# Kernel tuning notes

Hardware: AMD Instinct MI355X
Metric: run time of the kernel (lower is better)

## Reference

```python
import jax, jax.numpy as jnp
import numpy as np
from jax import lax

PS = 2  # patch_size
DN = ('NCHW', 'OIHW', 'NCHW')


def setup_inputs() -> dict:
    key = jax.random.key(0)
    ks = jax.random.split(key, 7)
    B, C, H, W = 8, 32, 512, 512
    return {
        'x': jax.random.normal(ks[0], (B, C, H, W), dtype=jnp.float32),
        'mlp_w': jax.random.normal(ks[1], (1, 1), dtype=jnp.float32),
        'mlp_b': jax.random.normal(ks[2], (1,), dtype=jnp.float32) * 0.1,
        'conv_w': jax.random.normal(ks[3], (C, 2 * C, 1, 1), dtype=jnp.float32) * (1.0 / np.sqrt(2 * C)),
        'conv_b': jax.random.normal(ks[4], (C,), dtype=jnp.float32) * 0.1,
        'convout_w': jax.random.normal(ks[5], (C, 2, 7, 7), dtype=jnp.float32) * (1.0 / np.sqrt(2 * 49)),
        'convout_b': jax.random.normal(ks[6], (C,), dtype=jnp.float32) * 0.1,
    }


def reference(x, mlp_w, mlp_b, conv_w, conv_b, convout_w, convout_b):
    B, C, H, W = x.shape
    hn, wn = H // PS, W // PS
    # Vectorized form of the per-patch Python loop:
    # blocks: (B, C, hn, PS, wn, PS)
    xb = x.reshape(B, C, hn, PS, wn, PS)
    m = jnp.max(xb, axis=(3, 5))   # (B, C, hn, wn) patch max pool
    a = jnp.mean(xb, axis=(3, 5))  # (B, C, hn, wn) patch avg pool
    # mlp(m) + mlp(a) with shared Linear(1,1): (m + a) * w + 2b
    gate = jax.nn.sigmoid((m + a) * mlp_w[0, 0] + 2.0 * mlp_b[0])
    product = (xb * gate[:, :, :, None, :, None]).reshape(B, C, H, W)
    # channel attention block
    cat = jnp.concatenate([product, x], axis=1)  # (B, 2C, H, W)
    out = lax.conv_general_dilated(cat, conv_w, (1, 1), 'SAME',
                                   dimension_numbers=DN) + conv_b[None, :, None, None]
    fs = out
    cm = jnp.max(out, axis=1, keepdims=True)   # channel max pool (B,1,H,W)
    ca = jnp.mean(out, axis=1, keepdims=True)  # channel avg pool (B,1,H,W)
    att = lax.conv_general_dilated(jnp.concatenate([cm, ca], axis=1), convout_w,
                                   (1, 1), 'SAME', dimension_numbers=DN)
    att = att + convout_b[None, :, None, None]
    return jax.nn.sigmoid(att) * fs
```

## Files before the change

### kernel.cpp

```cpp
#include <hip/hip_runtime.h>
#include <cstdint>
#include <cstddef>

constexpr int B = 8, C = 32, H = 512, W = 512;
constexpr int HW = H * W;

__device__ __forceinline__ float sigmoidf_(float z) {
    return 1.0f / (1.0f + __expf(-z));
}

__device__ __forceinline__ unsigned short bf16rne(float x) {
    unsigned int b = __float_as_uint(x);
    return (unsigned short)((b + 0x7FFFu + ((b >> 16) & 1u)) >> 16);
}
__device__ __forceinline__ float bf16tof(unsigned short h) {
    return __uint_as_float(((unsigned int)h) << 16);
}

typedef short s8v  __attribute__((ext_vector_type(8)));
typedef float f16v __attribute__((ext_vector_type(16)));

__global__ __launch_bounds__(256, 4) void k1_gate_conv(
    const float* __restrict__ x, const float* __restrict__ mlp_w,
    const float* __restrict__ mlp_b, const float* __restrict__ conv_w,
    const float* __restrict__ conv_b, float* __restrict__ fs,
    float* __restrict__ cm, float* __restrict__ ca)
{
    __shared__ float xs[32][256];
    __shared__ float gs[32][64];
    const int t  = threadIdx.x;
    const int c0 = blockIdx.x * 128;
    const int h0 = blockIdx.y * 2;
    const int b  = blockIdx.z;

    #pragma unroll
    for (int k = 0; k < 8; ++k) {
        int li = k * 256 + t;
        int c = li >> 6, q = li & 63;
        int p = q * 4;
        int row = p >> 7, col = p & 127;
        const float4 v = *(const float4*)(x + ((size_t)(b * C + c) * H + h0 + row) * W + c0 + col);
        *(float4*)&xs[c][p] = v;
    }
    __syncthreads();

    const float gw = mlp_w[0];
    const float gb = 2.0f * mlp_b[0];
    #pragma unroll
    for (int k = 0; k < 8; ++k) {
        int gi = k * 256 + t;
        int c = gi >> 6, wp = gi & 63;
        float a0 = xs[c][2 * wp],       a1 = xs[c][2 * wp + 1];
        float a2 = xs[c][128 + 2 * wp], a3 = xs[c][129 + 2 * wp];
        float mx = fmaxf(fmaxf(a0, a1), fmaxf(a2, a3));
        float av = 0.25f * ((a0 + a1) + (a2 + a3));
        gs[c][wp] = sigmoidf_(fmaf(mx + av, gw, gb));
    }
    __syncthreads();

    const int row = t >> 7, col = t & 127, wp = col >> 1;
    float xv[32], xg[32];
    #pragma unroll
    for (int c = 0; c < 32; ++c) {
        float v = xs[c][t];
        xv[c] = v;
        xg[c] = v * gs[c][wp];
    }
    float cmax = -3.4e38f, csum = 0.0f;
    const size_t pixoff = ((size_t)(b * C) * H + h0 + row) * W + c0 + col;
    #pragma unroll 4
    for (int o = 0; o < 32; ++o) {
        const float* wr = conv_w + o * 64;
        float acc0 = conv_b[o], acc1 = 0.0f;
        #pragma unroll
        for (int c = 0; c < 32; ++c) {
            acc0 = fmaf(xg[c], wr[c],      acc0);
            acc1 = fmaf(xv[c], wr[32 + c], acc1);
        }
        float acc = acc0 + acc1;
        fs[pixoff + (size_t)o * HW] = acc;
        cmax = fmaxf(cmax, acc);
        csum += acc;
    }
    const size_t pp = ((size_t)b * H + h0 + row) * W + c0 + col;
    cm[pp] = cmax;
    ca[pp] = csum * (1.0f / 32.0f);
}

__global__ __launch_bounds__(256, 3) void k2_conv7_mfma(
    const float* __restrict__ cm, const float* __restrict__ ca,
    const float* __restrict__ convout_w, const float* __restrict__ convout_b,
    float* __restrict__ io )
{
    __shared__ unsigned short win[4 * 14 * 144];
    const int t  = threadIdx.x;
    const int x0 = blockIdx.x * 128;
    const int y0 = blockIdx.y * 8;
    const int b  = blockIdx.z;

    #pragma unroll
    for (int k = 0; k < 16; ++k) {
        int n = k * 256 + t;
        if (n < 4032) {
            int j   = (n >= 2016) ? 1 : 0;
            int rem = n - j * 2016;
            int row = rem / 144;
            int col = rem - row * 144;
            int gy = y0 - 3 + row;
            int gx = x0 - 3 + col;
            float v = 0.0f;
            if ((unsigned)gy < (unsigned)H && (unsigned)gx < (unsigned)W)
                v = (j ? ca : cm)[(size_t)b * HW + (size_t)gy * W + gx];
            unsigned short hb = bf16rne(v);
            unsigned short lb = bf16rne(v - bf16tof(hb));
            win[n]        = hb;
            win[n + 4032] = lb;
        }
    }

    const int l  = t & 63;
    const int wv = t >> 6;
    const int o  = l & 31;
    const int j  = l >> 5;
    s8v whi[7], wlo[7];
    #pragma unroll
    for (int dy = 0; dy < 7; ++dy) {
        #pragma unroll
        for (int q = 0; q < 8; ++q) {
            float wf = (q < 7) ? convout_w[(o * 2 + j) * 49 + dy * 7 + q] : 0.0f;
            unsigned short hb = bf16rne(wf);
            unsigned short lb = bf16rne(wf - bf16tof(hb));
            whi[dy][q] = (short)hb;
            wlo[dy][q] = (short)lb;
        }
    }
    float bias[16];
    #pragma unroll
    for (int r = 0; r < 16; ++r)
        bias[r] = convout_b[(r & 3) + 8 * (r >> 2) + 4 * j];
    __syncthreads();

    const int xl  = wv * 32 + o;
    const int q0  = xl >> 1;
    const bool odd = (xl & 1) != 0;

    #pragma unroll 1
    for (int y = 0; y < 8; ++y) {
        f16v acc;
        #pragma unroll
        for (int r = 0; r < 16; ++r) acc[r] = bias[r];

        #pragma unroll
        for (int dy = 0; dy < 7; ++dy) {
            const unsigned int* rp =
                (const unsigned int*)win + (size_t)(y + dy) * 72 + j * 1008 + q0;
            unsigned int d0 = rp[0], d1 = rp[1], d2 = rp[2], d3 = rp[3], d4 = rp[4];
            const unsigned int* rp2 = rp + 2016;
            unsigned int e0 = rp2[0], e1 = rp2[1], e2 = rp2[2], e3 = rp2[3], e4 = rp2[4];

            union { unsigned int u[4]; s8v s; } Bh, Bl;
            if (odd) {
                Bh.u[0] = (d0 >> 16) | (d1 << 16);
                Bh.u[1] = (d1 >> 16) | (d2 << 16);
                Bh.u[2] = (d2 >> 16) | (d3 << 16);
                Bh.u[3] = (d3 >> 16) | (d4 << 16);
                Bl.u[0] = (e0 >> 16) | (e1 << 16);
                Bl.u[1] = (e1 >> 16) | (e2 << 16);
                Bl.u[2] = (e2 >> 16) | (e3 << 16);
                Bl.u[3] = (e3 >> 16) | (e4 << 16);
            } else {
                Bh.u[0] = d0; Bh.u[1] = d1; Bh.u[2] = d2; Bh.u[3] = d3;
                Bl.u[0] = e0; Bl.u[1] = e1; Bl.u[2] = e2; Bl.u[3] = e3;
            }
            acc = __builtin_amdgcn_mfma_f32_32x32x16_bf16(whi[dy], Bh.s, acc, 0, 0, 0);
            acc = __builtin_amdgcn_mfma_f32_32x32x16_bf16(whi[dy], Bl.s, acc, 0, 0, 0);
            acc = __builtin_amdgcn_mfma_f32_32x32x16_bf16(wlo[dy], Bh.s, acc, 0, 0, 0);
        }

        const int Y = y0 + y;
        const int X = x0 + xl;
        #pragma unroll
        for (int r = 0; r < 16; ++r) {
            int oc = (r & 3) + 8 * (r >> 2) + 4 * j;
            size_t a = ((size_t)(b * C + oc) * H + Y) * W + X;
            float f = io[a];
            io[a] = f * sigmoidf_(acc[r]);
        }
    }
}

extern "C" void kernel_launch(void* const* d_in, const int* in_sizes, int n_in,
                              void* d_out, int out_size, void* d_ws, size_t ws_size,
                              hipStream_t stream)
{
    const float* x         = (const float*)d_in[0];
    const float* mlp_w     = (const float*)d_in[1];
    const float* mlp_b     = (const float*)d_in[2];
    const float* conv_w    = (const float*)d_in[3];
    const float* conv_b    = (const float*)d_in[4];
    const float* convout_w = (const float*)d_in[5];
    const float* convout_b = (const float*)d_in[6];

    float* out = (float*)d_out;
    float* cm  = (float*)d_ws;
    float* ca  = cm + (size_t)B * HW;

    k1_gate_conv<<<dim3(4, 256, 8), 256, 0, stream>>>(
        x, mlp_w, mlp_b, conv_w, conv_b, out, cm, ca);
    k2_conv7_mfma<<<dim3(4, 64, 8), 256, 0, stream>>>(
        cm, ca, convout_w, convout_b, out);
}
```

Baseline: 616.4 us.

## Move 1x1 channel conv in k1 onto split-bf16 MFMA with direct-to-LDS loads

```diff
diff --git a/kernel.cpp b/kernel.cpp
--- a/kernel.cpp
+++ b/kernel.cpp
@@ -9,82 +9,148 @@
     return 1.0f / (1.0f + __expf(-z));
 }
 
-__device__ __forceinline__ unsigned short bf16rne(float x) {
+__device__ __forceinline__ unsigned int bf16rne(float x) {
     unsigned int b = __float_as_uint(x);
-    return (unsigned short)((b + 0x7FFFu + ((b >> 16) & 1u)) >> 16);
-}
-__device__ __forceinline__ float bf16tof(unsigned short h) {
-    return __uint_as_float(((unsigned int)h) << 16);
-}
+    return (b + 0x7FFFu + ((b >> 16) & 1u)) >> 16;
+}
+__device__ __forceinline__ float bf16tof(unsigned int h) {
+    return __uint_as_float(h << 16);
+}
+
+typedef uint2 __attribute__((may_alias)) uint2_ma;
+
+__device__ __forceinline__ void split4(float a, float b2, float c, float d,
+                                       uint2& hi, uint2& lo) {
+    unsigned ha = bf16rne(a), hb = bf16rne(b2), hc = bf16rne(c), hd = bf16rne(d);
+    unsigned la = bf16rne(a - bf16tof(ha)), lb = bf16rne(b2 - bf16tof(hb));
+    unsigned lc = bf16rne(c - bf16tof(hc)), ld = bf16rne(d - bf16tof(hd));
+    hi = make_uint2(ha | (hb << 16), hc | (hd << 16));
+    lo = make_uint2(la | (lb << 16), lc | (ld << 16));
+}
+
+typedef __attribute__((address_space(1))) const void gv_t;
+typedef __attribute__((address_space(3))) void lv_t;
 
 typedef short s8v  __attribute__((ext_vector_type(8)));
 typedef float f16v __attribute__((ext_vector_type(16)));
 
-__global__ __launch_bounds__(256, 4) void k1_gate_conv(
+__global__ __launch_bounds__(256, 4) void k1_gate_conv_mfma(
     const float* __restrict__ x, const float* __restrict__ mlp_w,
     const float* __restrict__ mlp_b, const float* __restrict__ conv_w,
     const float* __restrict__ conv_b, float* __restrict__ fs,
     float* __restrict__ cm, float* __restrict__ ca)
 {
-    __shared__ float xs[32][256];
-    __shared__ float gs[32][64];
+    __shared__ float xs[32][128];
+    __shared__ float gs[32][32];
+    __shared__ unsigned short Bb[4][2304];
+
     const int t  = threadIdx.x;
-    const int c0 = blockIdx.x * 128;
+    const int l  = t & 63;
+    const int wv = t >> 6;
+    const int x0 = blockIdx.x * 64;
     const int h0 = blockIdx.y * 2;
     const int b  = blockIdx.z;
 
     #pragma unroll
-    for (int k = 0; k < 8; ++k) {
-        int li = k * 256 + t;
-        int c = li >> 6, q = li & 63;
-        int p = q * 4;
-        int row = p >> 7, col = p & 127;
-        const float4 v = *(const float4*)(x + ((size_t)(b * C + c) * H + h0 + row) * W + c0 + col);
-        *(float4*)&xs[c][p] = v;
-    }
+    for (int i = 0; i < 4; ++i) {
+        const int m   = wv * 4 + i;
+        const int f   = m * 256 + l * 4;
+        const int c   = f >> 7;
+        const int px  = f & 127;
+        const int row = px >> 6, col = px & 63;
+        const float* src = x + ((size_t)(b * C + c) * H + h0 + row) * W + x0 + col;
+        float* dst = &xs[0][0] + m * 256;
+        __builtin_amdgcn_global_load_lds((gv_t*)src, (lv_t*)dst, 16, 0, 0);
+    }
+
+    const int o = l & 31;
+    const int j = l >> 5;
+    s8v whi[4], wlo[4];
+    #pragma unroll
+    for (int s = 0; s < 4; ++s) {
+        #pragma unroll
+        for (int q = 0; q < 8; ++q) {
+            float wf = conv_w[o * 64 + 16 * s + 8 * j + q];
+            unsigned hb = bf16rne(wf);
+            whi[s][q] = (short)hb;
+            wlo[s][q] = (short)bf16rne(wf - bf16tof(hb));
+        }
+    }
+    f16v acc;
+    #pragma unroll
+    for (int r = 0; r < 16; ++r) acc[r] = conv_b[(r & 3) + 8 * (r >> 2) + 4 * j];
+
     __syncthreads();
 
     const float gw = mlp_w[0];
     const float gb = 2.0f * mlp_b[0];
     #pragma unroll
-    for (int k = 0; k < 8; ++k) {
-        int gi = k * 256 + t;
-        int c = gi >> 6, wp = gi & 63;
-        float a0 = xs[c][2 * wp],       a1 = xs[c][2 * wp + 1];
-        float a2 = xs[c][128 + 2 * wp], a3 = xs[c][129 + 2 * wp];
-        float mx = fmaxf(fmaxf(a0, a1), fmaxf(a2, a3));
-        float av = 0.25f * ((a0 + a1) + (a2 + a3));
+    for (int it = 0; it < 4; ++it) {
+        int gi = it * 256 + t;
+        int c = gi >> 5, wp = gi & 31;
+        float2 fa = *(const float2*)&xs[c][2 * wp];
+        float2 fb = *(const float2*)&xs[c][64 + 2 * wp];
+        float mx = fmaxf(fmaxf(fa.x, fa.y), fmaxf(fb.x, fb.y));
+        float av = 0.25f * ((fa.x + fa.y) + (fb.x + fb.y));
         gs[c][wp] = sigmoidf_(fmaf(mx + av, gw, gb));
     }
     __syncthreads();
 
-    const int row = t >> 7, col = t & 127, wp = col >> 1;
-    float xv[32], xg[32];
-    #pragma unroll
-    for (int c = 0; c < 32; ++c) {
-        float v = xs[c][t];
-        xv[c] = v;
-        xg[c] = v * gs[c][wp];
-    }
-    float cmax = -3.4e38f, csum = 0.0f;
-    const size_t pixoff = ((size_t)(b * C) * H + h0 + row) * W + c0 + col;
-    #pragma unroll 4
-    for (int o = 0; o < 32; ++o) {
-        const float* wr = conv_w + o * 64;
-        float acc0 = conv_b[o], acc1 = 0.0f;
-        #pragma unroll
-        for (int c = 0; c < 32; ++c) {
-            acc0 = fmaf(xg[c], wr[c],      acc0);
-            acc1 = fmaf(xv[c], wr[32 + c], acc1);
-        }
-        float acc = acc0 + acc1;
-        fs[pixoff + (size_t)o * HW] = acc;
-        cmax = fmaxf(cmax, acc);
-        csum += acc;
-    }
-    const size_t pp = ((size_t)b * H + h0 + row) * W + c0 + col;
-    cm[pp] = cmax;
-    ca[pp] = csum * (1.0f / 32.0f);
+    const int q4   = l & 7;
+    const int pxb  = 4 * q4;
+    const int wp0  = 16 * (wv & 1) + 2 * q4;
+    const int xoff = (wv >> 1) * 64 + 32 * (wv & 1) + pxb;
+    const int cgrp = l >> 3;
+
+    #pragma unroll
+    for (int half = 0; half < 2; ++half) {
+        #pragma unroll
+        for (int cc = 0; cc < 2; ++cc) {
+            const int kr = 2 * cgrp + cc;
+            const int c  = 16 * half + kr;
+            const float4 v = *(const float4*)&xs[c][xoff];
+            const float2 g = *(const float2*)&gs[c][wp0];
+            uint2 hi, lo;
+            split4(v.x * g.x, v.y * g.x, v.z * g.y, v.w * g.y, hi, lo);
+            *(uint2_ma*)&Bb[wv][kr * 36 + pxb]        = hi;
+            *(uint2_ma*)&Bb[wv][576 + kr * 36 + pxb]  = lo;
+            split4(v.x, v.y, v.z, v.w, hi, lo);
+            *(uint2_ma*)&Bb[wv][1152 + kr * 36 + pxb] = hi;
+            *(uint2_ma*)&Bb[wv][1728 + kr * 36 + pxb] = lo;
+        }
+        #pragma unroll
+        for (int qq = 0; qq < 2; ++qq) {
+            const int s  = 2 * qq + half;
+            const int fb = qq * 1152 + 288 * j + (l & 31);
+            s8v fh, fl;
+            #pragma unroll
+            for (int q = 0; q < 8; ++q) {
+                fh[q] = (short)Bb[wv][fb + 36 * q];
+                fl[q] = (short)Bb[wv][fb + 576 + 36 * q];
+            }
+            acc = __builtin_amdgcn_mfma_f32_32x32x16_bf16(whi[s], fh, acc, 0, 0, 0);
+            acc = __builtin_amdgcn_mfma_f32_32x32x16_bf16(whi[s], fl, acc, 0, 0, 0);
+            acc = __builtin_amdgcn_mfma_f32_32x32x16_bf16(wlo[s], fh, acc, 0, 0, 0);
+        }
+    }
+
+    const int gy = h0 + (wv >> 1);
+    const int gx = x0 + 32 * (wv & 1) + (l & 31);
+    float cmx = -3.4e38f, csm = 0.0f;
+    #pragma unroll
+    for (int r = 0; r < 16; ++r) {
+        const int oc = (r & 3) + 8 * (r >> 2) + 4 * j;
+        fs[((size_t)(b * C + oc) * H + gy) * W + gx] = acc[r];
+        cmx = fmaxf(cmx, acc[r]);
+        csm += acc[r];
+    }
+    cmx = fmaxf(cmx, __shfl_xor(cmx, 32));
+    csm += __shfl_xor(csm, 32);
+    if (l < 32) {
+        const size_t pp = ((size_t)b * H + gy) * W + gx;
+        cm[pp] = cmx;
+        ca[pp] = csm * (1.0f / 32.0f);
+    }
 }
 
 __global__ __launch_bounds__(256, 3) void k2_conv7_mfma(
@@ -111,10 +177,10 @@
             float v = 0.0f;
             if ((unsigned)gy < (unsigned)H && (unsigned)gx < (unsigned)W)
                 v = (j ? ca : cm)[(size_t)b * HW + (size_t)gy * W + gx];
-            unsigned short hb = bf16rne(v);
-            unsigned short lb = bf16rne(v - bf16tof(hb));
-            win[n]        = hb;
-            win[n + 4032] = lb;
+            unsigned hb = bf16rne(v);
+            unsigned lb = bf16rne(v - bf16tof(hb));
+            win[n]        = (unsigned short)hb;
+            win[n + 4032] = (unsigned short)lb;
         }
     }
 
@@ -128,8 +194,8 @@
         #pragma unroll
         for (int q = 0; q < 8; ++q) {
             float wf = (q < 7) ? convout_w[(o * 2 + j) * 49 + dy * 7 + q] : 0.0f;
-            unsigned short hb = bf16rne(wf);
-            unsigned short lb = bf16rne(wf - bf16tof(hb));
+            unsigned hb = bf16rne(wf);
+            unsigned lb = bf16rne(wf - bf16tof(hb));
             whi[dy][q] = (short)hb;
             wlo[dy][q] = (short)lb;
         }
@@ -205,7 +271,7 @@
     float* cm  = (float*)d_ws;
     float* ca  = cm + (size_t)B * HW;
 
-    k1_gate_conv<<<dim3(4, 256, 8), 256, 0, stream>>>(
+    k1_gate_conv_mfma<<<dim3(8, 256, 8), 256, 0, stream>>>(
         x, mlp_w, mlp_b, conv_w, conv_b, out, cm, ca);
     k2_conv7_mfma<<<dim3(4, 64, 8), 256, 0, stream>>>(
         cm, ca, convout_w, convout_b, out);
```

New measurement: 592.9 us. 3.8% less time.
